# Performance work log

Hardware: AMD Instinct MI355X
Metric: run time of the kernel (lower is better)

Reference implementation:

```python
import jax, jax.numpy as jnp
import numpy as np

B, T, D, K = 8, 2048, 768, 2048

def setup_inputs() -> dict:
    key = jax.random.key(0)
    k1, k2 = jax.random.split(key)
    token = jax.random.normal(k1, (B, T, D), dtype=jnp.float32)
    codebook = jax.random.normal(k2, (K, D), dtype=jnp.float32)
    return {"token": token, "codebook": codebook}

def reference(token, codebook):
    x_sq = jnp.sum(token * token, axis=-1, keepdims=True)          # [B,T,1]
    e_sq = jnp.sum(codebook * codebook, axis=-1)                   # [K]
    dots = jnp.einsum('btd,kd->btk', token, codebook)              # [B,T,K]
    dist = x_sq - 2.0 * dots + e_sq                                # [B,T,K]
    indices = jnp.argmin(dist, axis=-1)                            # [B,T] int
    quantize = codebook[indices]                                   # [B,T,D] gather
    # commitment loss: mse(sg(quantize), x)
    commit_loss = jnp.mean(jnp.square(jax.lax.stop_gradient(quantize) - token))
    # straight-through estimator
    quantized = token + jax.lax.stop_gradient(quantize - token)
    return quantized, indices, commit_loss
```

## Files before the change

kernel.cpp:

```cpp
#include <hip/hip_runtime.h>

#define M_TOK 16384
#define D_DIM 768
#define K_CB  2048

#define BTOK  128
#define BCODE 128
#define BK    32
#define KSPLIT 4
#define SLICE (K_CB / KSPLIT)
#define NCT   (SLICE / BCODE)
#define NSLOT (KSPLIT * 2)
#define EPS   0.25f

typedef __attribute__((ext_vector_type(8))) short bf16x8;
typedef __attribute__((ext_vector_type(4))) float f32x4;

__device__ __forceinline__ unsigned short f2bf(float x) {
    unsigned u = __float_as_uint(x);
    return (unsigned short)((u + 0x7fffu + ((u >> 16) & 1u)) >> 16);
}
__device__ __forceinline__ float bf2f(unsigned short h) {
    return __uint_as_float((unsigned)h << 16);
}

#define ASYNC16(gp, lp) __builtin_amdgcn_global_load_lds( \
    (const __attribute__((address_space(1))) void*)(gp),  \
    (__attribute__((address_space(3))) void*)(lp), 16, 0, 0)

__global__ void vq_prep(const float* __restrict__ cb,
                        unsigned short* __restrict__ cb_hi,
                        unsigned short* __restrict__ cb_lo,
                        float* __restrict__ esq) {
    const int w = threadIdx.x >> 6, lane = threadIdx.x & 63;
    const int k = blockIdx.x * 4 + w;
    const float* row = cb + (size_t)k * D_DIM;
    unsigned short* hk = cb_hi + (size_t)k * D_DIM;
    unsigned short* lk = cb_lo + (size_t)k * D_DIM;
    float s = 0.f;
    for (int j = lane; j < D_DIM; j += 64) {
        float x = row[j];
        s = fmaf(x, x, s);
        unsigned short h = f2bf(x);
        hk[j] = h;
        lk[j] = f2bf(x - bf2f(h));
    }
    #pragma unroll
    for (int off = 32; off; off >>= 1) s += __shfl_down(s, off);
    if (!lane) esq[k] = s;
}

__launch_bounds__(256, 2)
__global__ void vq_dist_mfma(const float* __restrict__ token,
                             const unsigned short* __restrict__ cb_hi,
                             const unsigned short* __restrict__ cb_lo,
                             const float* __restrict__ esq,
                             float4* __restrict__ top2) {
    __shared__ unsigned short sAh[BCODE][BK];
    __shared__ unsigned short sAl[BCODE][BK];
    __shared__ unsigned short sBh[BTOK][BK];
    __shared__ unsigned short sBl[BTOK][BK];
    __shared__ float esq_s[SLICE];

    const int tid  = threadIdx.x;
    const int lane = tid & 63;
    const int w    = tid >> 6;
    const int tokBase    = blockIdx.x * BTOK;
    const int kSliceBase = blockIdx.y * SLICE;

    for (int j = tid; j < SLICE; j += 256) esq_s[j] = esq[kSliceBase + j];

    const int wc = (w >> 1) * 64;
    const int wt = (w & 1) * 64;
    const int lm = lane & 15;
    const int lk = (lane >> 4) * 8;

    float rm1[4], rm2[4];
    int   rk1[4], rk2[4];
    #pragma unroll
    for (int j = 0; j < 4; ++j) {
        rm1[j] = 3.4e38f; rm2[j] = 3.4e38f;
        rk1[j] = 0x7fffffff; rk2[j] = 0x7fffffff;
    }

    for (int ct = 0; ct < NCT; ++ct) {
        const int codeBase = kSliceBase + ct * BCODE;

        f32x4 acc[4][4];
        #pragma unroll
        for (int i = 0; i < 4; ++i)
            #pragma unroll
            for (int j = 0; j < 4; ++j) acc[i][j] = (f32x4){0.f, 0.f, 0.f, 0.f};

        for (int dc = 0; dc < D_DIM; dc += BK) {
            __syncthreads();
            float4 tv[4];
            #pragma unroll
            for (int j = 0; j < 4; ++j) {
                const int idx = j * 256 + tid;
                const int r = idx >> 3, c4 = idx & 7;
                tv[j] = *(const float4*)(token + (size_t)(tokBase + r) * D_DIM + dc + c4 * 4);
            }
            #pragma unroll
            for (int q = 0; q < 2; ++q) {
                const int i = w * 128 + q * 64 + lane;
                const int r = i >> 2, seg = i & 3;
                const size_t goff = (size_t)(codeBase + r) * D_DIM + dc + seg * 8;
                ASYNC16(cb_hi + goff, (char*)&sAh[0][0] + i * 16);
                ASYNC16(cb_lo + goff, (char*)&sAl[0][0] + i * 16);
            }
            #pragma unroll
            for (int j = 0; j < 4; ++j) {
                const int idx = j * 256 + tid;
                const int r = idx >> 3, c4 = idx & 7;
                const unsigned short h0 = f2bf(tv[j].x), h1 = f2bf(tv[j].y),
                                     h2 = f2bf(tv[j].z), h3 = f2bf(tv[j].w);
                const unsigned short l0 = f2bf(tv[j].x - bf2f(h0)),
                                     l1 = f2bf(tv[j].y - bf2f(h1)),
                                     l2 = f2bf(tv[j].z - bf2f(h2)),
                                     l3 = f2bf(tv[j].w - bf2f(h3));
                uint2 ph, pl;
                ph.x = (unsigned)h0 | ((unsigned)h1 << 16);
                ph.y = (unsigned)h2 | ((unsigned)h3 << 16);
                pl.x = (unsigned)l0 | ((unsigned)l1 << 16);
                pl.y = (unsigned)l2 | ((unsigned)l3 << 16);
                *(uint2*)&sBh[r][c4 * 4] = ph;
                *(uint2*)&sBl[r][c4 * 4] = pl;
            }
            __syncthreads();

            bf16x8 ah[4], al[4], bh[4], bl[4];
            #pragma unroll
            for (int i = 0; i < 4; ++i) {
                ah[i] = *(const bf16x8*)&sAh[wc + i * 16 + lm][lk];
                al[i] = *(const bf16x8*)&sAl[wc + i * 16 + lm][lk];
            }
            #pragma unroll
            for (int j = 0; j < 4; ++j) {
                bh[j] = *(const bf16x8*)&sBh[wt + j * 16 + lm][lk];
                bl[j] = *(const bf16x8*)&sBl[wt + j * 16 + lm][lk];
            }
            #pragma unroll
            for (int i = 0; i < 4; ++i)
                #pragma unroll
                for (int j = 0; j < 4; ++j) {
                    acc[i][j] = __builtin_amdgcn_mfma_f32_16x16x32_bf16(ah[i], bh[j], acc[i][j], 0, 0, 0);
                    acc[i][j] = __builtin_amdgcn_mfma_f32_16x16x32_bf16(ah[i], bl[j], acc[i][j], 0, 0, 0);
                    acc[i][j] = __builtin_amdgcn_mfma_f32_16x16x32_bf16(al[i], bh[j], acc[i][j], 0, 0, 0);
                }
        }

        #pragma unroll
        for (int j = 0; j < 4; ++j)
            #pragma unroll
            for (int i = 0; i < 4; ++i)
                #pragma unroll
                for (int r = 0; r < 4; ++r) {
                    const int cl = ct * BCODE + wc + i * 16 + (lane >> 4) * 4 + r;
                    const float s = esq_s[cl] - 2.0f * acc[i][j][r];
                    const int kg = kSliceBase + cl;
                    if (s < rm1[j]) {
                        rm2[j] = rm1[j]; rk2[j] = rk1[j];
                        rm1[j] = s;      rk1[j] = kg;
                    } else if (s < rm2[j]) {
                        rm2[j] = s; rk2[j] = kg;
                    }
                }
    }

    #pragma unroll
    for (int j = 0; j < 4; ++j) {
        float m1 = rm1[j], m2 = rm2[j];
        int   k1 = rk1[j], k2 = rk2[j];
        #pragma unroll
        for (int off = 16; off <= 32; off <<= 1) {
            const float om1 = __shfl_xor(m1, off); const int ok1 = __shfl_xor(k1, off);
            const float om2 = __shfl_xor(m2, off); const int ok2 = __shfl_xor(k2, off);
            const bool aB = (m1 < om1) || (m1 == om1 && k1 < ok1);
            float n1m, n2m; int n1k, n2k;
            if (aB) {
                n1m = m1; n1k = k1;
                const bool t = (om1 < m2) || (om1 == m2 && ok1 < k2);
                n2m = t ? om1 : m2; n2k = t ? ok1 : k2;
            } else {
                n1m = om1; n1k = ok1;
                const bool t = (m1 < om2) || (m1 == om2 && k1 < ok2);
                n2m = t ? m1 : om2; n2k = t ? k1 : ok2;
            }
            m1 = n1m; k1 = n1k; m2 = n2m; k2 = n2k;
        }
        if (lane < 16) {
            const int t = tokBase + wt + j * 16 + lane;
            const int slot = blockIdx.y * 2 + (w >> 1);
            top2[(size_t)t * NSLOT + slot] =
                make_float4(m1, __int_as_float(k1), m2, __int_as_float(k2));
        }
    }
}

__global__ void vq_rescore(const float* __restrict__ token,
                           const float* __restrict__ cb,
                           const float* __restrict__ esq,
                           const float4* __restrict__ top2,
                           unsigned int* __restrict__ idx_out) {
    const int w = threadIdx.x >> 6, lane = threadIdx.x & 63;
    const int t = blockIdx.x * 4 + w;
    const float4* slots = top2 + (size_t)t * NSLOT;

    float4 s0 = slots[0];
    float m1 = s0.x, m2 = s0.z;
    int   k1 = __float_as_int(s0.y), k2 = __float_as_int(s0.w);
    #pragma unroll
    for (int s = 1; s < NSLOT; ++s) {
        const float4 sv = slots[s];
        const float om1 = sv.x, om2 = sv.z;
        const int ok1 = __float_as_int(sv.y), ok2 = __float_as_int(sv.w);
        const bool aB = (m1 < om1) || (m1 == om1 && k1 < ok1);
        float n1m, n2m; int n1k, n2k;
        if (aB) {
            n1m = m1; n1k = k1;
            const bool c = (om1 < m2) || (om1 == m2 && ok1 < k2);
            n2m = c ? om1 : m2; n2k = c ? ok1 : k2;
        } else {
            n1m = om1; n1k = ok1;
            const bool c = (m1 < om2) || (m1 == om2 && k1 < ok2);
            n2m = c ? m1 : om2; n2k = c ? k1 : ok2;
        }
        m1 = n1m; k1 = n1k; m2 = n2m; k2 = n2k;
    }

    unsigned choice = (unsigned)k1;
    if (!(m2 - m1 > EPS)) {
        const float* tr = token + (size_t)t * D_DIM;
        const float* c1 = cb + (size_t)k1 * D_DIM;
        const float* c2 = cb + (size_t)k2 * D_DIM;
        float d1 = 0.f, d2 = 0.f;
        for (int e = lane; e < D_DIM; e += 64) {
            const float x = tr[e];
            d1 = fmaf(c1[e], x, d1);
            d2 = fmaf(c2[e], x, d2);
        }
        #pragma unroll
        for (int off = 32; off; off >>= 1) {
            d1 += __shfl_down(d1, off);
            d2 += __shfl_down(d2, off);
        }
        d1 = __shfl(d1, 0);
        d2 = __shfl(d2, 0);
        const float s1 = esq[k1] - 2.f * d1;
        const float s2 = esq[k2] - 2.f * d2;
        if (s2 < s1 || (s2 == s1 && k2 < k1)) choice = (unsigned)k2;
    }
    if (!lane) idx_out[t] = choice;
}

__global__ void vq_gather(const float* __restrict__ token,
                          const float* __restrict__ cb,
                          const unsigned int* __restrict__ idx_in,
                          float* __restrict__ out_q,
                          float* __restrict__ out_idx,
                          float* __restrict__ out_loss) {
    const int gid = blockIdx.x * blockDim.x + threadIdx.x;
    const int nthreads = gridDim.x * blockDim.x;
    const int N4 = (M_TOK * D_DIM) / 4;
    float lsum = 0.f;
    for (int i = gid; i < N4; i += nthreads) {
        const int t  = i / 192;
        const int c4 = (i - t * 192) * 4;
        const int idx = (int)idx_in[t];
        const float4 q = *(const float4*)(cb + (size_t)idx * D_DIM + c4);
        const float4 x = *(const float4*)(token + (size_t)t * D_DIM + c4);
        const float dx = q.x - x.x, dy = q.y - x.y, dz = q.z - x.z, dw = q.w - x.w;
        lsum += dx * dx + dy * dy + dz * dz + dw * dw;
        *(float4*)(out_q + (size_t)t * D_DIM + c4) = q;
    }
    if (gid < M_TOK) out_idx[gid] = (float)idx_in[gid];

    #pragma unroll
    for (int off = 32; off; off >>= 1) lsum += __shfl_down(lsum, off);
    __shared__ float ws[4];
    const int lane = threadIdx.x & 63, wid = threadIdx.x >> 6;
    if (lane == 0) ws[wid] = lsum;
    __syncthreads();
    if (threadIdx.x == 0)
        atomicAdd(out_loss, (ws[0] + ws[1] + ws[2] + ws[3]) *
                            (1.0f / (float)((size_t)M_TOK * D_DIM)));
}

extern "C" void kernel_launch(void* const* d_in, const int* in_sizes, int n_in,
                              void* d_out, int out_size, void* d_ws, size_t ws_size,
                              hipStream_t stream) {
    const float* token = (const float*)d_in[0];
    const float* cb    = (const float*)d_in[1];

    float* out_q    = (float*)d_out;
    float* out_idx  = out_q + (size_t)M_TOK * D_DIM;
    float* out_loss = out_idx + M_TOK;

    char* w = (char*)d_ws;
    unsigned short* cb_hi = (unsigned short*)(w);
    unsigned short* cb_lo = (unsigned short*)(w + 3145728);
    float*          esq   = (float*)(w + 6291456);
    float4*         top2  = (float4*)(w + 6299648);
    unsigned int*   idxb  = (unsigned int*)(w + 8396800);

    hipMemsetAsync(out_loss, 0, sizeof(float), stream);

    vq_prep<<<K_CB / 4, 256, 0, stream>>>(cb, cb_hi, cb_lo, esq);

    dim3 g(M_TOK / BTOK, KSPLIT);
    vq_dist_mfma<<<g, 256, 0, stream>>>(token, cb_hi, cb_lo, esq, top2);

    vq_rescore<<<M_TOK / 4, 256, 0, stream>>>(token, cb, esq, top2, idxb);

    vq_gather<<<2048, 256, 0, stream>>>(token, cb, idxb,
                                        out_q, out_idx, out_loss);
}
```

Before: 315.0 us.

## Pre-split tokens to bf16, swizzle LDS, raise split-K, fuse rescore with gather

Adds a pre-pass that splits tokens into bf16 hi/lo arrays, stored in the output buffer as scratch, so the distance kernel loads both operands with async global-to-LDS copies instead of converting fp32 tokens every K step. It applies an XOR swizzle to the LDS layout to cut bank conflicts, doubles the codebook split to 8 with a flattened grid, and raises launch bounds to 4 blocks per CU. The rescore and gather kernels are merged into one per-token kernel that reduces the 16 slots with shuffles. In exchange it adds an extra token-sized read and write pass, and it depends on out_q being overwritten after the distance kernel has consumed the scratch.

```diff
diff --git a/kernel.cpp b/kernel.cpp
--- a/kernel.cpp
+++ b/kernel.cpp
@@ -7,7 +7,7 @@
 #define BTOK  128
 #define BCODE 128
 #define BK    32
-#define KSPLIT 4
+#define KSPLIT 8
 #define SLICE (K_CB / KSPLIT)
 #define NCT   (SLICE / BCODE)
 #define NSLOT (KSPLIT * 2)
@@ -28,10 +28,10 @@
     (const __attribute__((address_space(1))) void*)(gp),  \
     (__attribute__((address_space(3))) void*)(lp), 16, 0, 0)
 
-__global__ void vq_prep(const float* __restrict__ cb,
-                        unsigned short* __restrict__ cb_hi,
-                        unsigned short* __restrict__ cb_lo,
-                        float* __restrict__ esq) {
+__global__ void vq_prep_cb(const float* __restrict__ cb,
+                           unsigned short* __restrict__ cb_hi,
+                           unsigned short* __restrict__ cb_lo,
+                           float* __restrict__ esq) {
     const int w = threadIdx.x >> 6, lane = threadIdx.x & 63;
     const int k = blockIdx.x * 4 + w;
     const float* row = cb + (size_t)k * D_DIM;
@@ -50,30 +50,79 @@
     if (!lane) esq[k] = s;
 }
 
-__launch_bounds__(256, 2)
-__global__ void vq_dist_mfma(const float* __restrict__ token,
+__global__ void vq_prep_tok(const float* __restrict__ tok,
+                            unsigned short* __restrict__ th,
+                            unsigned short* __restrict__ tl) {
+    const int N8 = (M_TOK * D_DIM) / 8;
+    const int stride = gridDim.x * blockDim.x;
+    for (int i = blockIdx.x * blockDim.x + threadIdx.x; i < N8; i += stride) {
+        const float4 a = *(const float4*)(tok + (size_t)i * 8);
+        const float4 b = *(const float4*)(tok + (size_t)i * 8 + 4);
+        const float v[8] = {a.x, a.y, a.z, a.w, b.x, b.y, b.z, b.w};
+        unsigned hh[8], ll[8];
+        #pragma unroll
+        for (int j = 0; j < 8; ++j) {
+            const unsigned short h = f2bf(v[j]);
+            hh[j] = h;
+            ll[j] = f2bf(v[j] - bf2f(h));
+        }
+        uint4 ph, pl;
+        ph.x = hh[0] | (hh[1] << 16);  ph.y = hh[2] | (hh[3] << 16);
+        ph.z = hh[4] | (hh[5] << 16);  ph.w = hh[6] | (hh[7] << 16);
+        pl.x = ll[0] | (ll[1] << 16);  pl.y = ll[2] | (ll[3] << 16);
+        pl.z = ll[4] | (ll[5] << 16);  pl.w = ll[6] | (ll[7] << 16);
+        *(uint4*)(th + (size_t)i * 8) = ph;
+        *(uint4*)(tl + (size_t)i * 8) = pl;
+    }
+}
+
+__launch_bounds__(256, 4)
+__global__ void vq_dist_mfma(const unsigned short* __restrict__ tok_hi,
+                             const unsigned short* __restrict__ tok_lo,
                              const unsigned short* __restrict__ cb_hi,
                              const unsigned short* __restrict__ cb_lo,
                              const float* __restrict__ esq,
                              float4* __restrict__ top2) {
-    __shared__ unsigned short sAh[BCODE][BK];
-    __shared__ unsigned short sAl[BCODE][BK];
-    __shared__ unsigned short sBh[BTOK][BK];
-    __shared__ unsigned short sBl[BTOK][BK];
+    __shared__ unsigned short sAh[BCODE * BK];
+    __shared__ unsigned short sAl[BCODE * BK];
+    __shared__ unsigned short sBh[BTOK * BK];
+    __shared__ unsigned short sBl[BTOK * BK];
     __shared__ float esq_s[SLICE];
 
     const int tid  = threadIdx.x;
     const int lane = tid & 63;
     const int w    = tid >> 6;
-    const int tokBase    = blockIdx.x * BTOK;
-    const int kSliceBase = blockIdx.y * SLICE;
+
+    const int bid = blockIdx.x;
+    const int ksl = bid & 7;
+    const int txi = bid >> 3;
+    const int tokBase    = txi * BTOK;
+    const int kSliceBase = ksl * SLICE;
 
     for (int j = tid; j < SLICE; j += 256) esq_s[j] = esq[kSliceBase + j];
 
+    int gOff[2], gLds[2];
+    #pragma unroll
+    for (int q = 0; q < 2; ++q) {
+        const int G   = w * 128 + q * 64 + lane;
+        const int row = G >> 2;
+        const int hs  = (G & 3) ^ ((row >> 1) & 3);
+        gOff[q] = (row * D_DIM + hs * 8) * 2;
+        gLds[q] = G * 16;
+    }
+
+    const int h  = lane >> 4;
+    const int lm = lane & 15;
     const int wc = (w >> 1) * 64;
     const int wt = (w & 1) * 64;
-    const int lm = lane & 15;
-    const int lk = (lane >> 4) * 8;
+    int offA[4], offB[4];
+    #pragma unroll
+    for (int i = 0; i < 4; ++i) {
+        const int rA = wc + i * 16 + lm;
+        offA[i] = rA * 64 + ((h ^ ((rA >> 1) & 3)) * 16);
+        const int rB = wt + i * 16 + lm;
+        offB[i] = rB * 64 + ((h ^ ((rB >> 1) & 3)) * 16);
+    }
 
     float rm1[4], rm2[4];
     int   rk1[4], rk2[4];
@@ -83,8 +132,13 @@
         rk1[j] = 0x7fffffff; rk2[j] = 0x7fffffff;
     }
 
+    const char* pBh = (const char*)(tok_hi + (size_t)tokBase * D_DIM);
+    const char* pBl = (const char*)(tok_lo + (size_t)tokBase * D_DIM);
+
     for (int ct = 0; ct < NCT; ++ct) {
         const int codeBase = kSliceBase + ct * BCODE;
+        const char* pAh = (const char*)(cb_hi + (size_t)codeBase * D_DIM);
+        const char* pAl = (const char*)(cb_lo + (size_t)codeBase * D_DIM);
 
         f32x4 acc[4][4];
         #pragma unroll
@@ -93,52 +147,27 @@
             for (int j = 0; j < 4; ++j) acc[i][j] = (f32x4){0.f, 0.f, 0.f, 0.f};
 
         for (int dc = 0; dc < D_DIM; dc += BK) {
+            const int dcb = dc * 2;
             __syncthreads();
-            float4 tv[4];
-            #pragma unroll
-            for (int j = 0; j < 4; ++j) {
-                const int idx = j * 256 + tid;
-                const int r = idx >> 3, c4 = idx & 7;
-                tv[j] = *(const float4*)(token + (size_t)(tokBase + r) * D_DIM + dc + c4 * 4);
-            }
             #pragma unroll
             for (int q = 0; q < 2; ++q) {
-                const int i = w * 128 + q * 64 + lane;
-                const int r = i >> 2, seg = i & 3;
-                const size_t goff = (size_t)(codeBase + r) * D_DIM + dc + seg * 8;
-                ASYNC16(cb_hi + goff, (char*)&sAh[0][0] + i * 16);
-                ASYNC16(cb_lo + goff, (char*)&sAl[0][0] + i * 16);
-            }
-            #pragma unroll
-            for (int j = 0; j < 4; ++j) {
-                const int idx = j * 256 + tid;
-                const int r = idx >> 3, c4 = idx & 7;
-                const unsigned short h0 = f2bf(tv[j].x), h1 = f2bf(tv[j].y),
-                                     h2 = f2bf(tv[j].z), h3 = f2bf(tv[j].w);
-                const unsigned short l0 = f2bf(tv[j].x - bf2f(h0)),
-                                     l1 = f2bf(tv[j].y - bf2f(h1)),
-                                     l2 = f2bf(tv[j].z - bf2f(h2)),
-                                     l3 = f2bf(tv[j].w - bf2f(h3));
-                uint2 ph, pl;
-                ph.x = (unsigned)h0 | ((unsigned)h1 << 16);
-                ph.y = (unsigned)h2 | ((unsigned)h3 << 16);
-                pl.x = (unsigned)l0 | ((unsigned)l1 << 16);
-                pl.y = (unsigned)l2 | ((unsigned)l3 << 16);
-                *(uint2*)&sBh[r][c4 * 4] = ph;
-                *(uint2*)&sBl[r][c4 * 4] = pl;
+                ASYNC16(pAh + gOff[q] + dcb, (char*)sAh + gLds[q]);
+                ASYNC16(pAl + gOff[q] + dcb, (char*)sAl + gLds[q]);
+                ASYNC16(pBh + gOff[q] + dcb, (char*)sBh + gLds[q]);
+                ASYNC16(pBl + gOff[q] + dcb, (char*)sBl + gLds[q]);
             }
             __syncthreads();
 
             bf16x8 ah[4], al[4], bh[4], bl[4];
             #pragma unroll
             for (int i = 0; i < 4; ++i) {
-                ah[i] = *(const bf16x8*)&sAh[wc + i * 16 + lm][lk];
-                al[i] = *(const bf16x8*)&sAl[wc + i * 16 + lm][lk];
+                ah[i] = *(const bf16x8*)((const char*)sAh + offA[i]);
+                al[i] = *(const bf16x8*)((const char*)sAl + offA[i]);
             }
             #pragma unroll
             for (int j = 0; j < 4; ++j) {
-                bh[j] = *(const bf16x8*)&sBh[wt + j * 16 + lm][lk];
-                bl[j] = *(const bf16x8*)&sBl[wt + j * 16 + lm][lk];
+                bh[j] = *(const bf16x8*)((const char*)sBh + offB[j]);
+                bl[j] = *(const bf16x8*)((const char*)sBl + offB[j]);
             }
             #pragma unroll
             for (int i = 0; i < 4; ++i)
@@ -191,30 +220,30 @@
         }
         if (lane < 16) {
             const int t = tokBase + wt + j * 16 + lane;
-            const int slot = blockIdx.y * 2 + (w >> 1);
+            const int slot = ksl * 2 + (w >> 1);
             top2[(size_t)t * NSLOT + slot] =
                 make_float4(m1, __int_as_float(k1), m2, __int_as_float(k2));
         }
     }
 }
 
-__global__ void vq_rescore(const float* __restrict__ token,
-                           const float* __restrict__ cb,
-                           const float* __restrict__ esq,
-                           const float4* __restrict__ top2,
-                           unsigned int* __restrict__ idx_out) {
+__global__ void vq_final(const float* __restrict__ token,
+                         const float* __restrict__ cb,
+                         const float* __restrict__ esq,
+                         const float4* __restrict__ top2,
+                         float* __restrict__ out_q,
+                         float* __restrict__ out_idx,
+                         float* __restrict__ out_loss) {
     const int w = threadIdx.x >> 6, lane = threadIdx.x & 63;
     const int t = blockIdx.x * 4 + w;
-    const float4* slots = top2 + (size_t)t * NSLOT;
-
-    float4 s0 = slots[0];
-    float m1 = s0.x, m2 = s0.z;
-    int   k1 = __float_as_int(s0.y), k2 = __float_as_int(s0.w);
-    #pragma unroll
-    for (int s = 1; s < NSLOT; ++s) {
-        const float4 sv = slots[s];
-        const float om1 = sv.x, om2 = sv.z;
-        const int ok1 = __float_as_int(sv.y), ok2 = __float_as_int(sv.w);
+
+    const float4 sv = top2[(size_t)t * NSLOT + (lane & 15)];
+    float m1 = sv.x, m2 = sv.z;
+    int   k1 = __float_as_int(sv.y), k2 = __float_as_int(sv.w);
+    #pragma unroll
+    for (int off = 1; off <= 8; off <<= 1) {
+        const float om1 = __shfl_xor(m1, off); const int ok1 = __shfl_xor(k1, off);
+        const float om2 = __shfl_xor(m2, off); const int ok2 = __shfl_xor(k2, off);
         const bool aB = (m1 < om1) || (m1 == om1 && k1 < ok1);
         float n1m, n2m; int n1k, n2k;
         if (aB) {
@@ -251,39 +280,29 @@
         const float s2 = esq[k2] - 2.f * d2;
         if (s2 < s1 || (s2 == s1 && k2 < k1)) choice = (unsigned)k2;
     }
-    if (!lane) idx_out[t] = choice;
-}
-
-__global__ void vq_gather(const float* __restrict__ token,
-                          const float* __restrict__ cb,
-                          const unsigned int* __restrict__ idx_in,
-                          float* __restrict__ out_q,
-                          float* __restrict__ out_idx,
-                          float* __restrict__ out_loss) {
-    const int gid = blockIdx.x * blockDim.x + threadIdx.x;
-    const int nthreads = gridDim.x * blockDim.x;
-    const int N4 = (M_TOK * D_DIM) / 4;
+
+    const float* crow = cb + (size_t)choice * D_DIM;
+    const float* trow = token + (size_t)t * D_DIM;
+    float*       qrow = out_q + (size_t)t * D_DIM;
     float lsum = 0.f;
-    for (int i = gid; i < N4; i += nthreads) {
-        const int t  = i / 192;
-        const int c4 = (i - t * 192) * 4;
-        const int idx = (int)idx_in[t];
-        const float4 q = *(const float4*)(cb + (size_t)idx * D_DIM + c4);
-        const float4 x = *(const float4*)(token + (size_t)t * D_DIM + c4);
+    #pragma unroll
+    for (int u = 0; u < 3; ++u) {
+        const int e = (u * 64 + lane) * 4;
+        const float4 q = *(const float4*)(crow + e);
+        const float4 x = *(const float4*)(trow + e);
+        *(float4*)(qrow + e) = q;
         const float dx = q.x - x.x, dy = q.y - x.y, dz = q.z - x.z, dw = q.w - x.w;
         lsum += dx * dx + dy * dy + dz * dz + dw * dw;
-        *(float4*)(out_q + (size_t)t * D_DIM + c4) = q;
-    }
-    if (gid < M_TOK) out_idx[gid] = (float)idx_in[gid];
+    }
+    if (!lane) out_idx[t] = (float)choice;
 
     #pragma unroll
     for (int off = 32; off; off >>= 1) lsum += __shfl_down(lsum, off);
-    __shared__ float ws[4];
-    const int lane = threadIdx.x & 63, wid = threadIdx.x >> 6;
-    if (lane == 0) ws[wid] = lsum;
+    __shared__ float ws4[4];
+    if (!lane) ws4[w] = lsum;
     __syncthreads();
-    if (threadIdx.x == 0)
-        atomicAdd(out_loss, (ws[0] + ws[1] + ws[2] + ws[3]) *
+    if (!threadIdx.x)
+        atomicAdd(out_loss, (ws4[0] + ws4[1] + ws4[2] + ws4[3]) *
                             (1.0f / (float)((size_t)M_TOK * D_DIM)));
 }
 
@@ -297,22 +316,23 @@
     float* out_idx  = out_q + (size_t)M_TOK * D_DIM;
     float* out_loss = out_idx + M_TOK;
 
-    char* w = (char*)d_ws;
-    unsigned short* cb_hi = (unsigned short*)(w);
-    unsigned short* cb_lo = (unsigned short*)(w + 3145728);
-    float*          esq   = (float*)(w + 6291456);
-    float4*         top2  = (float4*)(w + 6299648);
-    unsigned int*   idxb  = (unsigned int*)(w + 8396800);
+    unsigned short* tok_hi = (unsigned short*)out_q;
+    unsigned short* tok_lo = tok_hi + (size_t)M_TOK * D_DIM;
+
+    char* ws = (char*)d_ws;
+    unsigned short* cb_hi = (unsigned short*)(ws);
+    unsigned short* cb_lo = (unsigned short*)(ws + 3145728);
+    float*          esq   = (float*)(ws + 6291456);
+    float4*         top2  = (float4*)(ws + 6299648);
 
     hipMemsetAsync(out_loss, 0, sizeof(float), stream);
 
-    vq_prep<<<K_CB / 4, 256, 0, stream>>>(cb, cb_hi, cb_lo, esq);
-
-    dim3 g(M_TOK / BTOK, KSPLIT);
-    vq_dist_mfma<<<g, 256, 0, stream>>>(token, cb_hi, cb_lo, esq, top2);
-
-    vq_rescore<<<M_TOK / 4, 256, 0, stream>>>(token, cb, esq, top2, idxb);
-
-    vq_gather<<<2048, 256, 0, stream>>>(token, cb, idxb,
-                                        out_q, out_idx, out_loss);
-}
+    vq_prep_cb<<<K_CB / 4, 256, 0, stream>>>(cb, cb_hi, cb_lo, esq);
+    vq_prep_tok<<<3072, 256, 0, stream>>>(token, tok_hi, tok_lo);
+
+    vq_dist_mfma<<<(M_TOK / BTOK) * KSPLIT, 256, 0, stream>>>(
+        tok_hi, tok_lo, cb_hi, cb_lo, esq, top2);
+
+    vq_final<<<M_TOK / 4, 256, 0, stream>>>(token, cb, esq, top2,
+                                            out_q, out_idx, out_loss);
+}
```

Result: slower. 348.1 us (+10.5%).
